# Kernel tuning notes

Hardware: AMD Instinct MI355X
Metric: run time of the kernel (lower is better)

## Reference

```python
import jax, jax.numpy as jnp
import numpy as np
from jax import lax

B, T, H, IN = 2048, 2048, 25, 1


def setup_inputs() -> dict:
    key = jax.random.key(0)
    ks = jax.random.split(key, 7)
    s = 1.0 / np.sqrt(H)  # PyTorch LSTM init scale
    return {
        "x": jax.random.normal(ks[0], (B, T, IN), dtype=jnp.float32),
        "w_ih": jax.random.uniform(ks[1], (4 * H, IN), jnp.float32, -s, s),
        "w_hh": jax.random.uniform(ks[2], (4 * H, H), jnp.float32, -s, s),
        "b_ih": jax.random.uniform(ks[3], (4 * H,), jnp.float32, -s, s),
        "b_hh": jax.random.uniform(ks[4], (4 * H,), jnp.float32, -s, s),
        "w_dense": jax.random.uniform(ks[5], (1, H), jnp.float32, -s, s),
        "b_dense": jax.random.uniform(ks[6], (1,), jnp.float32, -s, s),
    }


def reference(x, w_ih, w_hh, b_ih, b_hh, w_dense, b_dense):
    # x: [B, T, 1] -> scan over time on [T, B, *]
    xt = jnp.swapaxes(x, 0, 1)                     # [T, B, IN]
    x_proj = xt @ w_ih.T + (b_ih + b_hh)           # [T, B, 4H], input projection precomputed

    def step(carry, xp):
        h, c = carry
        gates = xp + h @ w_hh.T                    # [B, 4H]
        i, f, g, o = jnp.split(gates, 4, axis=-1)  # PyTorch gate order i,f,g,o
        i = jax.nn.sigmoid(i)
        f = jax.nn.sigmoid(f)
        g = jnp.tanh(g)
        o = jax.nn.sigmoid(o)
        c = f * c + i * g
        h = o * jnp.tanh(c)
        return (h, c), h

    h0 = jnp.zeros((x.shape[0], H), dtype=x.dtype)
    c0 = jnp.zeros((x.shape[0], H), dtype=x.dtype)
    _, hs = lax.scan(step, (h0, c0), x_proj)       # hs: [T, B, H]
    hs = jnp.swapaxes(hs, 0, 1)                    # [B, T, H]
    return hs @ w_dense.T + b_dense                # [B, T, 1]
```

## Files before the change

kernel.cpp:

```cpp
#include <hip/hip_runtime.h>

#define T_LEN 2048
#define HID   25
#define LOG2E 1.4426950408889634f

typedef float vf4 __attribute__((vector_size(16), may_alias));
typedef float f2  __attribute__((ext_vector_type(2)));

__device__ __forceinline__ float fast_rcp(float x) { return __builtin_amdgcn_rcpf(x); }
__device__ __forceinline__ float fast_exp2(float x) { return __builtin_amdgcn_exp2f(x); }


__global__ __attribute__((amdgpu_flat_work_group_size(256, 256),
                          amdgpu_waves_per_eu(1, 1)))
void lstm_fused(
    const float* __restrict__ x,
    const float* __restrict__ w_ih,
    const float* __restrict__ w_hh,
    const float* __restrict__ b_ih,
    const float* __restrict__ b_hh,
    const float* __restrict__ w_dense,
    const float* __restrict__ b_dense,
    float* __restrict__ out)
{
    const int tid  = threadIdx.x;
    const int u    = tid & 31;
    const int cb   = tid >> 5;
    const int b    = blockIdx.x * 8 + cb;
    const bool act = u < HID;

    __shared__ __align__(16) float hbuf[8][32];
    __shared__ float hist[8][32][33];

    const float si = -LOG2E, sg = 2.f * LOG2E;

    f2 wI2[12], wF2[12], wG2[12], wO2[12];
#pragma unroll
    for (int m = 0; m < 12; ++m) {
        wI2[m] = act ? f2{si * w_hh[u * HID + m],             si * w_hh[u * HID + m + 12]}             : f2{0.f, 0.f};
        wF2[m] = act ? f2{si * w_hh[(HID + u) * HID + m],     si * w_hh[(HID + u) * HID + m + 12]}     : f2{0.f, 0.f};
        wG2[m] = act ? f2{sg * w_hh[(2 * HID + u) * HID + m], sg * w_hh[(2 * HID + u) * HID + m + 12]} : f2{0.f, 0.f};
        wO2[m] = act ? f2{si * w_hh[(3 * HID + u) * HID + m], si * w_hh[(3 * HID + u) * HID + m + 12]} : f2{0.f, 0.f};
    }
    const float wI24 = act ? si * w_hh[u * HID + 24]             : 0.f;
    const float wF24 = act ? si * w_hh[(HID + u) * HID + 24]     : 0.f;
    const float wG24 = act ? sg * w_hh[(2 * HID + u) * HID + 24] : 0.f;
    const float wO24 = act ? si * w_hh[(3 * HID + u) * HID + 24] : 0.f;

    const float bI  = act ? si * (b_ih[u] + b_hh[u]) : 0.f;
    const float bF  = act ? si * (b_ih[HID + u] + b_hh[HID + u]) : 0.f;
    const float bG  = act ? sg * (b_ih[2 * HID + u] + b_hh[2 * HID + u]) : 0.f;
    const float bO  = act ? si * (b_ih[3 * HID + u] + b_hh[3 * HID + u]) : 0.f;
    const float wxI = act ? si * w_ih[u] : 0.f;
    const float wxF = act ? si * w_ih[HID + u] : 0.f;
    const float wxG = act ? sg * w_ih[2 * HID + u] : 0.f;
    const float wxO = act ? si * w_ih[3 * HID + u] : 0.f;
    const float bd  = b_dense[0];

    float wdv[HID];
#pragma unroll
    for (int i = 0; i < HID; ++i) wdv[i] = w_dense[i];

    hbuf[cb][u] = 0.f;

    const int slot = (u < 12) ? 2 * u : (u < 24) ? 2 * u - 23 : u;
    float* hwr = &hbuf[cb][slot];
    const vf4* r4 = (const vf4*)&hbuf[cb][0];
    const float* hbF = &hbuf[cb][0];

    const float4* __restrict__ xp = (const float4*)(x + (size_t)b * T_LEN);
    float* __restrict__ orow = out + (size_t)b * T_LEN;

    f2 hp[12];
#pragma unroll
    for (int m = 0; m < 12; ++m) hp[m] = f2{0.f, 0.f};
    float h24 = 0.f;

    float c = 0.f;
    float4 xcur = xp[0];

    for (int it = 0; it < T_LEN / 4; ++it) {
        const int nx = (it + 1 < T_LEN / 4) ? it + 1 : it;
        float4 xnext = xp[nx];
        float xs[4] = {xcur.x, xcur.y, xcur.z, xcur.w};

#pragma unroll
        for (int s = 0; s < 4; ++s) {
            const float xv = xs[s];
            const int t = 4 * it + s;

            f2 accI = f2{fmaf(xv, wxI, bI), 0.f};
            f2 accF = f2{fmaf(xv, wxF, bF), 0.f};
            f2 accG = f2{fmaf(xv, wxG, bG), 0.f};
            f2 accO = f2{fmaf(xv, wxO, bO), 0.f};
#pragma unroll
            for (int m = 0; m < 12; ++m) {
                const f2 h = hp[m];
                accI = __builtin_elementwise_fma(h, wI2[m], accI);
                accF = __builtin_elementwise_fma(h, wF2[m], accF);
                accG = __builtin_elementwise_fma(h, wG2[m], accG);
                accO = __builtin_elementwise_fma(h, wO2[m], accO);
            }
            const float aI = accI.x + fmaf(h24, wI24, accI.y);
            const float aF = accF.x + fmaf(h24, wF24, accF.y);
            const float aG = accG.x + fmaf(h24, wG24, accG.y);
            const float aO = accO.x + fmaf(h24, wO24, accO.y);

            const float sI = fast_rcp(1.f + fast_exp2(aI));
            const float sF = fast_rcp(1.f + fast_exp2(aF));
            const float sO = fast_rcp(1.f + fast_exp2(aO));
            const float tG = fmaf(-2.f, fast_rcp(1.f + fast_exp2(aG)), 1.f);

            c = fmaf(sF, c, sI * tG);
            const float tC = fmaf(-2.f, fast_rcp(1.f + fast_exp2(2.f * LOG2E * c)), 1.f);
            const float hn = sO * tC;

            *hwr = hn;
            hist[cb][t & 31][u] = hn;
            __asm__ __volatile__("" ::: "memory");
            {
                vf4 a0 = r4[0], a1 = r4[1], a2 = r4[2];
                vf4 a3 = r4[3], a4 = r4[4], a5 = r4[5];
                hp[0]  = f2{a0[0], a0[1]}; hp[1]  = f2{a0[2], a0[3]};
                hp[2]  = f2{a1[0], a1[1]}; hp[3]  = f2{a1[2], a1[3]};
                hp[4]  = f2{a2[0], a2[1]}; hp[5]  = f2{a2[2], a2[3]};
                hp[6]  = f2{a3[0], a3[1]}; hp[7]  = f2{a3[2], a3[3]};
                hp[8]  = f2{a4[0], a4[1]}; hp[9]  = f2{a4[2], a4[3]};
                hp[10] = f2{a5[0], a5[1]}; hp[11] = f2{a5[2], a5[3]};
                h24 = hbF[24];
            }
            __asm__ __volatile__("" ::: "memory");

            if ((t & 31) == 31) {
                const float* hrow = &hist[cb][u][0];
                float ys = 0.f;
#pragma unroll
                for (int i = 0; i < HID; ++i)
                    ys = fmaf(hrow[i], wdv[i], ys);
                orow[(t & ~31) + u] = ys + bd;
            }
        }
        xcur = xnext;
    }
}

extern "C" void kernel_launch(void* const* d_in, const int* in_sizes, int n_in,
                              void* d_out, int out_size, void* d_ws, size_t ws_size,
                              hipStream_t stream) {
    const float* x       = (const float*)d_in[0];
    const float* w_ih    = (const float*)d_in[1];
    const float* w_hh    = (const float*)d_in[2];
    const float* b_ih    = (const float*)d_in[3];
    const float* b_hh    = (const float*)d_in[4];
    const float* w_dense = (const float*)d_in[5];
    const float* b_dense = (const float*)d_in[6];
    float* out = (float*)d_out;

    lstm_fused<<<dim3(256), dim3(256), 0, stream>>>(x, w_ih, w_hh, b_ih, b_hh,
                                                    w_dense, b_dense, out);
}
```

Baseline: 545.0 us.

## Compute dense projection per step from broadcast hidden state, drop history buffer

Removes the per-step write to the shared history buffer and the 32-step batched dense projection. Instead, every lane computes the dense output for the current step from the hidden vector it already reloaded, and the lane whose index matches the step keeps that value for a coalesced store every 32 steps. The 25th hidden element is folded into a 13th packed pair so the scalar tail FMA goes away, and inactive lanes write to a separate dummy row to avoid conflicts. The cost is 13 extra packed FMAs per step on every lane, in exchange for fewer LDS stores and no periodic 25-load reduction.

```diff
diff --git a/kernel.cpp b/kernel.cpp
--- a/kernel.cpp
+++ b/kernel.cpp
@@ -5,6 +5,7 @@
 #define LOG2E 1.4426950408889634f
 
 typedef float vf4 __attribute__((vector_size(16), may_alias));
+typedef float vf2 __attribute__((vector_size(8),  may_alias));
 typedef float f2  __attribute__((ext_vector_type(2)));
 
 __device__ __forceinline__ float fast_rcp(float x) { return __builtin_amdgcn_rcpf(x); }
@@ -29,12 +30,11 @@
     const int b    = blockIdx.x * 8 + cb;
     const bool act = u < HID;
 
-    __shared__ __align__(16) float hbuf[8][32];
-    __shared__ float hist[8][32][33];
+    __shared__ __align__(16) float hbuf[16][32];
 
     const float si = -LOG2E, sg = 2.f * LOG2E;
 
-    f2 wI2[12], wF2[12], wG2[12], wO2[12];
+    f2 wI2[13], wF2[13], wG2[13], wO2[13];
 #pragma unroll
     for (int m = 0; m < 12; ++m) {
         wI2[m] = act ? f2{si * w_hh[u * HID + m],             si * w_hh[u * HID + m + 12]}             : f2{0.f, 0.f};
@@ -42,10 +42,10 @@
         wG2[m] = act ? f2{sg * w_hh[(2 * HID + u) * HID + m], sg * w_hh[(2 * HID + u) * HID + m + 12]} : f2{0.f, 0.f};
         wO2[m] = act ? f2{si * w_hh[(3 * HID + u) * HID + m], si * w_hh[(3 * HID + u) * HID + m + 12]} : f2{0.f, 0.f};
     }
-    const float wI24 = act ? si * w_hh[u * HID + 24]             : 0.f;
-    const float wF24 = act ? si * w_hh[(HID + u) * HID + 24]     : 0.f;
-    const float wG24 = act ? sg * w_hh[(2 * HID + u) * HID + 24] : 0.f;
-    const float wO24 = act ? si * w_hh[(3 * HID + u) * HID + 24] : 0.f;
+    wI2[12] = act ? f2{si * w_hh[u * HID + 24], 0.f}             : f2{0.f, 0.f};
+    wF2[12] = act ? f2{si * w_hh[(HID + u) * HID + 24], 0.f}     : f2{0.f, 0.f};
+    wG2[12] = act ? f2{sg * w_hh[(2 * HID + u) * HID + 24], 0.f} : f2{0.f, 0.f};
+    wO2[12] = act ? f2{si * w_hh[(3 * HID + u) * HID + 24], 0.f} : f2{0.f, 0.f};
 
     const float bI  = act ? si * (b_ih[u] + b_hh[u]) : 0.f;
     const float bF  = act ? si * (b_ih[HID + u] + b_hh[HID + u]) : 0.f;
@@ -57,26 +57,28 @@
     const float wxO = act ? si * w_ih[3 * HID + u] : 0.f;
     const float bd  = b_dense[0];
 
-    float wdv[HID];
+    f2 wd2[13];
 #pragma unroll
-    for (int i = 0; i < HID; ++i) wdv[i] = w_dense[i];
+    for (int m = 0; m < 12; ++m) wd2[m] = f2{w_dense[m], w_dense[m + 12]};
+    wd2[12] = f2{w_dense[24], 0.f};
 
     hbuf[cb][u] = 0.f;
+    hbuf[8 + cb][u] = 0.f;
 
-    const int slot = (u < 12) ? 2 * u : (u < 24) ? 2 * u - 23 : u;
-    float* hwr = &hbuf[cb][slot];
+    const int slot = (u < 12) ? 2 * u : (u < 24) ? 2 * u - 23 : 24;
+    float* hwr = act ? &hbuf[cb][slot] : &hbuf[8 + cb][u];
     const vf4* r4 = (const vf4*)&hbuf[cb][0];
-    const float* hbF = &hbuf[cb][0];
+    const vf2* r2 = (const vf2*)&hbuf[cb][24];
 
     const float4* __restrict__ xp = (const float4*)(x + (size_t)b * T_LEN);
     float* __restrict__ orow = out + (size_t)b * T_LEN;
 
-    f2 hp[12];
+    f2 hp[13];
 #pragma unroll
-    for (int m = 0; m < 12; ++m) hp[m] = f2{0.f, 0.f};
-    float h24 = 0.f;
+    for (int m = 0; m < 13; ++m) hp[m] = f2{0.f, 0.f};
 
     float c = 0.f;
+    float yroll = 0.f;
     float4 xcur = xp[0];
 
     for (int it = 0; it < T_LEN / 4; ++it) {
@@ -94,17 +96,17 @@
             f2 accG = f2{fmaf(xv, wxG, bG), 0.f};
             f2 accO = f2{fmaf(xv, wxO, bO), 0.f};
 #pragma unroll
-            for (int m = 0; m < 12; ++m) {
+            for (int m = 0; m < 13; ++m) {
                 const f2 h = hp[m];
                 accI = __builtin_elementwise_fma(h, wI2[m], accI);
                 accF = __builtin_elementwise_fma(h, wF2[m], accF);
                 accG = __builtin_elementwise_fma(h, wG2[m], accG);
                 accO = __builtin_elementwise_fma(h, wO2[m], accO);
             }
-            const float aI = accI.x + fmaf(h24, wI24, accI.y);
-            const float aF = accF.x + fmaf(h24, wF24, accF.y);
-            const float aG = accG.x + fmaf(h24, wG24, accG.y);
-            const float aO = accO.x + fmaf(h24, wO24, accO.y);
+            const float aI = accI.x + accI.y;
+            const float aF = accF.x + accF.y;
+            const float aG = accG.x + accG.y;
+            const float aO = accO.x + accO.y;
 
             const float sI = fast_rcp(1.f + fast_exp2(aI));
             const float sF = fast_rcp(1.f + fast_exp2(aF));
@@ -116,28 +118,29 @@
             const float hn = sO * tC;
 
             *hwr = hn;
-            hist[cb][t & 31][u] = hn;
             __asm__ __volatile__("" ::: "memory");
             {
                 vf4 a0 = r4[0], a1 = r4[1], a2 = r4[2];
                 vf4 a3 = r4[3], a4 = r4[4], a5 = r4[5];
+                vf2 a6 = r2[0];
                 hp[0]  = f2{a0[0], a0[1]}; hp[1]  = f2{a0[2], a0[3]};
                 hp[2]  = f2{a1[0], a1[1]}; hp[3]  = f2{a1[2], a1[3]};
                 hp[4]  = f2{a2[0], a2[1]}; hp[5]  = f2{a2[2], a2[3]};
                 hp[6]  = f2{a3[0], a3[1]}; hp[7]  = f2{a3[2], a3[3]};
                 hp[8]  = f2{a4[0], a4[1]}; hp[9]  = f2{a4[2], a4[3]};
                 hp[10] = f2{a5[0], a5[1]}; hp[11] = f2{a5[2], a5[3]};
-                h24 = hbF[24];
+                hp[12] = f2{a6[0], a6[1]};
             }
-            __asm__ __volatile__("" ::: "memory");
 
-            if ((t & 31) == 31) {
-                const float* hrow = &hist[cb][u][0];
-                float ys = 0.f;
+            {
+                f2 accY = f2{0.f, 0.f};
 #pragma unroll
-                for (int i = 0; i < HID; ++i)
-                    ys = fmaf(hrow[i], wdv[i], ys);
-                orow[(t & ~31) + u] = ys + bd;
+                for (int m = 0; m < 13; ++m)
+                    accY = __builtin_elementwise_fma(hp[m], wd2[m], accY);
+                const float ys = accY.x + accY.y;
+                yroll = ((t & 31) == u) ? ys : yroll;
+                if ((t & 31) == 31)
+                    orow[(t & ~31) + u] = yroll + bd;
             }
         }
         xcur = xnext;
```

Result: slower. 592.1 us (+8.6%).
